# Kernel tuning notes

Measured on AMD Instinct MI355X. Metric: run time of the kernel, lower is better.

Reference implementation:

```python
import jax, jax.numpy as jnp
import numpy as np

B, C, H, W = 2, 128, 128, 128
HEADS = 8
D = C // HEADS
EPS = 1e-5


def _conv(x, w, pad):
    # x: [B,C,H,W], w: [O,I,kh,kw]
    return jax.lax.conv_general_dilated(
        x, w, window_strides=(1, 1), padding=[(pad, pad), (pad, pad)],
        dimension_numbers=("NCHW", "OIHW", "NCHW"))


def setup_inputs() -> dict:
    key = jax.random.key(0)
    ks = jax.random.split(key, 9)
    s = 0.05
    w11 = lambda k: jax.random.normal(k, (C, C, 1, 1), jnp.float32) * s
    w33 = lambda k: jax.random.normal(k, (C, C, 3, 3), jnp.float32) * s
    return {
        "x": jax.random.normal(ks[0], (B, C, H, W), jnp.float32),
        "gamma": jnp.ones((W,), jnp.float32),   # LayerNorm over LAST dim (W==C)
        "beta": jnp.zeros((W,), jnp.float32),
        "scale": jnp.ones((1,), jnp.float32),
        "wq1": w11(ks[1]), "wq2": w33(ks[2]),
        "wk1": w11(ks[3]), "wk2": w33(ks[4]),
        "wv1": w11(ks[5]), "wv2": w33(ks[6]),
        "wo": w11(ks[7]),
    }


def reference(x, gamma, beta, scale, wq1, wq2, wk1, wk2, wv1, wv2, wo):
    residual = x
    # torch nn.LayerNorm(channels) normalizes the last axis (W), biased variance
    mu = jnp.mean(x, axis=-1, keepdims=True)
    var = jnp.var(x, axis=-1, keepdims=True)
    xn = (x - mu) * jax.lax.rsqrt(var + EPS) * gamma + beta

    q = _conv(_conv(xn, wq1, 0), wq2, 1).reshape(B, HEADS, H * W, D)
    k = _conv(_conv(xn, wk1, 0), wk2, 1).reshape(B, HEADS, H * W, D).transpose(0, 1, 3, 2)
    v = _conv(_conv(xn, wv1, 0), wv2, 1).reshape(B, HEADS, H * W, D)

    # transposed (channel) attention: [B,h,d,HW] @ [B,h,HW,d] -> [B,h,d,d]
    attn = jnp.matmul(k, q) / scale
    probs = jax.nn.softmax(attn, axis=-1)
    out = jnp.matmul(v, probs)                      # [B,h,HW,d]
    out = out.transpose(0, 1, 3, 2).reshape(B, C, H, W)
    return _conv(out, wo, 0) + residual
```

## Files before the change

kernel.cpp:

```cpp
#include <hip/hip_runtime.h>
#include <hip/hip_bf16.h>

typedef unsigned short u16;
typedef _Float16 f16;
typedef f16 f16x8 __attribute__((ext_vector_type(8)));
typedef float f32x4 __attribute__((ext_vector_type(4)));

__device__ __forceinline__ float b2f(u16 u) {
  unsigned v = (unsigned)u << 16; float f; __builtin_memcpy(&f, &v, 4); return f;
}
__device__ __forceinline__ u16 f2b(float f) {
  return __builtin_bit_cast(u16, __float2bfloat16(f));
}
__device__ __forceinline__ float h2f(u16 u) {
  return (float)__builtin_bit_cast(f16, u);
}
__device__ __forceinline__ u16 f2h(float f) {
  return __builtin_bit_cast(u16, (f16)f);
}
__device__ __forceinline__ void gload16(const void* g, void* l) {
  __builtin_amdgcn_global_load_lds((__attribute__((address_space(1))) void*)(const_cast<void*>(g)),
                                   (__attribute__((address_space(3))) void*)l, 16, 0, 0);
}
__device__ __forceinline__ f32x4 mfma16(int4 a, int4 b, f32x4 c) {
  return __builtin_amdgcn_mfma_f32_16x16x32_f16(__builtin_bit_cast(f16x8, a),
                                                __builtin_bit_cast(f16x8, b), c, 0, 0, 0);
}
union PK { int4 i; u16 u[8]; };

__device__ __forceinline__ int detect_isf(const u16* x, int tid, int nthr) {
  __shared__ int dcnt;
  if (tid == 0) dcnt = 0;
  __syncthreads();
  int c = 0;
  for (int i = tid; i < 1024; i += nthr) {
    u16 u = x[i * 2];
    if (((u >> 7) & 0xFF) >= 0x90) ++c;
  }
  if (c) atomicAdd(&dcnt, c);
  __syncthreads();
  return dcnt > 16;
}

#define XROW 33280

__global__ __launch_bounds__(256) void k_weff(
    const void* __restrict__ w1q, const void* __restrict__ w2q,
    const void* __restrict__ w1k, const void* __restrict__ w2k,
    const void* __restrict__ w1v, const void* __restrict__ w2v,
    const u16* __restrict__ xdet, u16* __restrict__ weff) {
  __shared__ __align__(16) u16 sA[16384];
  __shared__ __align__(16) u16 sB[16384];
  int tid = threadIdx.x;
  int isf = detect_isf(xdet, tid, 256);
  int blk = blockIdx.x;
  int tap = blk / 3, br = blk - tap * 3;
  const void* w1 = br == 0 ? w1q : (br == 1 ? w1k : w1v);
  const void* w2 = br == 0 ? w2q : (br == 1 ? w2k : w2v);
  if (isf) {
    const float* w2f = (const float*)w2;
    const float* w1f = (const float*)w1;
#pragma unroll 4
    for (int i = 0; i < 64; ++i) {
      int e = i * 256 + tid;
      int c = e >> 7, m = e & 127;
      sA[c * 128 + (m ^ ((c & 15) << 3))] = f2h(w2f[e * 9 + tap]);
      int ci = e & 127;
      sB[ci * 128 + ((e >> 7) ^ ((ci & 15) << 3))] = f2h(w1f[e]);
    }
  } else {
    const u16* w2u = (const u16*)w2;
    const u16* w1u = (const u16*)w1;
#pragma unroll 4
    for (int i = 0; i < 64; ++i) {
      int e = i * 256 + tid;
      int c = e >> 7, m = e & 127;
      sA[c * 128 + (m ^ ((c & 15) << 3))] = f2h(b2f(w2u[e * 9 + tap]));
      int ci = e & 127;
      sB[ci * 128 + ((e >> 7) ^ ((ci & 15) << 3))] = f2h(b2f(w1u[e]));
    }
  }
  __syncthreads();
  int lane = tid & 63, wv = tid >> 6;
  int m0w = (wv >> 1) * 64, n0w = (wv & 1) * 64;
  f32x4 acc[4][4] = {};
#pragma unroll
  for (int k0 = 0; k0 < 4; ++k0) {
    int mrow = k0 * 32 + (lane >> 4) * 8;
    int4 a4[4], b4[4];
#pragma unroll
    for (int mi = 0; mi < 4; ++mi) {
      int c = m0w + mi * 16 + (lane & 15);
      a4[mi] = *(const int4*)&sA[c * 128 + (mrow ^ ((c & 15) << 3))];
    }
#pragma unroll
    for (int ni = 0; ni < 4; ++ni) {
      int ci = n0w + ni * 16 + (lane & 15);
      b4[ni] = *(const int4*)&sB[ci * 128 + (mrow ^ ((ci & 15) << 3))];
    }
#pragma unroll
    for (int mi = 0; mi < 4; ++mi)
#pragma unroll
      for (int ni = 0; ni < 4; ++ni)
        acc[mi][ni] = mfma16(a4[mi], b4[ni], acc[mi][ni]);
  }
  __syncthreads();
#pragma unroll
  for (int mi = 0; mi < 4; ++mi)
#pragma unroll
    for (int ni = 0; ni < 4; ++ni) {
#pragma unroll
      for (int r = 0; r < 4; ++r) {
        int c = m0w + mi * 16 + (lane >> 4) * 4 + r;
        int ci = n0w + ni * 16 + (lane & 15);
        sA[c * 128 + ci] = f2h(acc[mi][ni][r]);
      }
    }
  __syncthreads();
  int4* dst = (int4*)((char*)weff + (size_t)blk * 32768);
#pragma unroll
  for (int i = 0; i < 8; ++i) {
    int gidx = i * 256 + tid;
    int k0 = gidx >> 9;
    int ch = gidx & 511;
    int mt = ch >> 6, l = ch & 63;
    int c = mt * 16 + (l & 15);
    int g = k0 * 4 + (l >> 4);
    dst[gidx] = *(const int4*)((const char*)sA + c * 256 + g * 16);
  }
}

__global__ __launch_bounds__(256) void k_ln(const void* __restrict__ xr,
    const void* __restrict__ gr, const void* __restrict__ br_,
    u16* __restrict__ xnt, float* __restrict__ attnb) {
  __shared__ __align__(16) float sx[16384];
  __shared__ __align__(16) u16 sn[16384];
  __shared__ float sg[128], sb[128];
  int tid = threadIdx.x;
  int bi = blockIdx.x;
  if (bi >= 256) {
    int pid = bi - 256;
    int b = pid >> 1, row = (pid & 1) ? 129 : 0;
    char* rbase = (char*)xnt + (size_t)(b * 130 + row) * XROW;
    int4 z = make_int4(0, 0, 0, 0);
    for (int i = 0; i < 9; ++i) {
      int idx = i * 256 + tid;
      if (idx < 2080) *(int4*)(rbase + idx * 16) = z;
    }
    return;
  }
  if (bi == 0) {
    for (int i = tid; i < 4096; i += 256) attnb[i] = 0.f;
  }
  int b = bi >> 7, h = bi & 127;
  int isf = detect_isf((const u16*)xr, tid, 256);
  if (tid < 128) {
    sg[tid] = isf ? ((const float*)gr)[tid] : b2f(((const u16*)gr)[tid]);
    sb[tid] = isf ? ((const float*)br_)[tid] : b2f(((const u16*)br_)[tid]);
  }
  if (isf) {
#pragma unroll
    for (int it = 0; it < 16; ++it) {
      int d = it * 4096 + tid * 16;
      int c = d >> 9;
      int p = (d >> 4) & 31;
      int sc = p ^ (c & 31);
      const char* src = (const char*)xr + (size_t)(b * 128 + c) * 65536 + (size_t)h * 512 + (sc << 4);
      gload16(src, (char*)sx + d);
    }
  } else {
    int c = tid >> 1, half = tid & 1;
    const u16* xu = (const u16*)xr + ((size_t)(b * 128 + c) * 128 + h) * 128 + half * 64;
    for (int i = 0; i < 16; ++i) {
      int phys = (half * 16 + i) ^ (c & 31);
      float* dst = sx + c * 128 + phys * 4;
#pragma unroll
      for (int j = 0; j < 4; ++j) dst[j] = b2f(xu[i * 4 + j]);
    }
  }
  __syncthreads();
  int c = tid >> 1, half = tid & 1;
  float sum = 0.f, sq = 0.f;
#pragma unroll
  for (int i = 0; i < 16; ++i) {
    int phys = (half * 16 + i) ^ (c & 31);
    const float* v = sx + c * 128 + phys * 4;
#pragma unroll
    for (int j = 0; j < 4; ++j) { float f = v[j]; sum += f; sq += f * f; }
  }
  sum += __shfl_xor(sum, 1);
  sq  += __shfl_xor(sq, 1);
  float mu = sum * 0.0078125f;
  float var = sq * 0.0078125f - mu * mu;
  float rs = rsqrtf(var + 1e-5f);
  int cg = c >> 3, cl = c & 7;
#pragma unroll
  for (int i = 0; i < 16; ++i) {
    int logical = half * 16 + i;
    int phys = logical ^ (c & 31);
    const float* v = sx + c * 128 + phys * 4;
#pragma unroll
    for (int j = 0; j < 4; ++j) {
      int w = logical * 4 + j;
      sn[w * 128 + (((cg ^ (w & 15)) << 3) | cl)] = f2h((v[j] - mu) * rs * sg[w] + sb[w]);
    }
  }
  __syncthreads();
  char* obase = (char*)xnt + (size_t)(b * 130 + h + 1) * XROW;
#pragma unroll
  for (int i = 0; i < 8; ++i) {
    int idx = i * 256 + tid;
    int g = idx >> 7, w = idx & 127;
    int phys = g ^ (w & 15);
    *(int4*)(obase + (g * 130 + w + 1) * 16) = *(const int4*)((const char*)sn + w * 256 + (phys << 4));
  }
  if (tid < 32) {
    int g = tid >> 1, side = tid & 1;
    *(int4*)(obase + (g * 130 + (side ? 129 : 0)) * 16) = make_int4(0, 0, 0, 0);
  }
}

#define STAGE_T(T, BUF) do { \
    const char* base_ = (const char*)weff + (size_t)(T) * 32768; \
    char* dst_ = wq + (BUF) * 32768; \
    _Pragma("unroll") \
    for (int i_ = 0; i_ < 8; ++i_) \
      gload16(base_ + i_ * 4096 + tid * 16, dst_ + i_ * 4096 + tid * 16); \
  } while (0)

#define BC_LOAD(DST, T6) do { \
    int dy_ = (T6) / 3, dx_ = (T6) % 3; \
    const char* rb_ = (const char*)xnt + (size_t)(b * 130 + h + dy_) * XROW; \
    _Pragma("unroll") \
    for (int kk = 0; kk < 4; ++kk) \
      _Pragma("unroll") \
      for (int ni = 0; ni < 2; ++ni) { \
        int wp1 = whalf * 64 + n0l + ni * 16 + (lane & 15) + dx_;    \
        int chunk = (kk * 4 + (lane >> 4)) * 130 + wp1; \
        DST[kk][ni] = *(const int4*)(rb_ + chunk * 16); \
      } \
  } while (0)

#define QFULL(ACC, QB) do { \
    _Pragma("unroll") \
    for (int k0 = 0; k0 < 4; ++k0) { \
      int4 af[4]; \
      _Pragma("unroll") \
      for (int mi = 0; mi < 4; ++mi) \
        af[mi] = *(const int4*)((QB) + k0 * 8192 + ((wv >> 1) * 4 + mi) * 1024 + lane * 16); \
      _Pragma("unroll") \
      for (int mi = 0; mi < 4; ++mi) { \
        ACC[mi][0] = mfma16(af[mi], bcA[k0][0], ACC[mi][0]); \
        ACC[mi][1] = mfma16(af[mi], bcA[k0][1], ACC[mi][1]); \
      } \
    } \
  } while (0)

__global__ __launch_bounds__(256, 2) void k_conv(const u16* __restrict__ xnt,
    const u16* __restrict__ weff, u16* __restrict__ Vc, float* __restrict__ attnb) {
  __shared__ __align__(16) char wq[65536];
  int tid = threadIdx.x, lane = tid & 63, wv = tid >> 6;
  int bi = blockIdx.x;
  int whalf = bi & 1, h = (bi >> 1) & 127, b = bi >> 8;
  int m0 = (wv >> 1) * 64;
  int n0l = (wv & 1) * 32;
  int r9 = bi % 9;

  int4 bcA[4][2], bcB[4][2];
  BC_LOAD(bcA, r9);
  STAGE_T(3 * r9, 0);
  __syncthreads();

  f32x4 aq[4][2] = {}, ak[4][2] = {}, av[4][2] = {};

  for (int t = 0; t < 27; ++t) {
    int br = t % 3, tgrp = t / 3;
    if (t + 1 < 27) {
      int tt1 = t + 1 + 3 * r9;
      if (tt1 >= 27) tt1 -= 27;
      STAGE_T(tt1, (t + 1) & 1);
    }
    if (br == 0) {
      if (tgrp > 0) {
#pragma unroll
        for (int kk = 0; kk < 4; ++kk)
#pragma unroll
          for (int ni = 0; ni < 2; ++ni) bcA[kk][ni] = bcB[kk][ni];
      }
      if (tgrp < 8) {
        int ntap = tgrp + 1 + r9;
        if (ntap >= 9) ntap -= 9;
        BC_LOAD(bcB, ntap);
      }
    }
    const char* qb = wq + (t & 1) * 32768;
    if (br == 0)      QFULL(aq, qb);
    else if (br == 1) QFULL(ak, qb);
    else              QFULL(av, qb);
    __syncthreads();
  }
  u16* scrQ = (u16*)wq;
  u16* scrK = (u16*)(wq + 16384);
  u16* scrV = (u16*)(wq + 32768);
#pragma unroll
  for (int mi = 0; mi < 4; ++mi)
#pragma unroll
    for (int ni = 0; ni < 2; ++ni)
#pragma unroll
      for (int r = 0; r < 4; ++r) {
        int cc = m0 + mi * 16 + (lane >> 4) * 4 + r;
        int wl = n0l + ni * 16 + (lane & 15);
        scrQ[cc * 64 + wl] = f2h(aq[mi][ni][r]);
        scrK[cc * 64 + wl] = f2h(ak[mi][ni][r]);
        scrV[cc * 64 + wl] = f2h(av[mi][ni][r]);
      }
  __syncthreads();
#pragma unroll
  for (int hh = 0; hh < 2; ++hh) {
    int hd = wv * 2 + hh;
    f32x4 g = {};
#pragma unroll
    for (int k2 = 0; k2 < 2; ++k2) {
      PK A, Bq;
#pragma unroll
      for (int jj = 0; jj < 8; ++jj) {
        int k = (lane >> 4) * 8 + jj;
        int ci = k2 * 8 + (k >> 2);
        int wl = (k & 3) * 16 + (lane & 15);
        A.u[jj]  = scrK[(hd * 16 + ci) * 64 + wl];
        Bq.u[jj] = scrQ[(hd * 16 + ci) * 64 + wl];
      }
      g = mfma16(A.i, Bq.i, g);
    }
#pragma unroll
    for (int r = 0; r < 4; ++r)
      atomicAdd(&attnb[((b * 8 + hd) * 16 + (lane >> 4) * 4 + r) * 16 + (lane & 15)], g[r]);
  }
  char* dstV = (char*)Vc + (size_t)(b * 128) * 32768 + (size_t)h * 256 + (size_t)whalf * 128;
#pragma unroll
  for (int i = 0; i < 4; ++i) {
    int gi = i * 256 + tid;
    int c = gi >> 3, off = (gi & 7) << 4;
    *(int4*)(dstV + (size_t)c * 32768 + off) = *(const int4*)((const char*)scrV + c * 128 + off);
  }
}

__global__ __launch_bounds__(256) void k_w2(const float* __restrict__ attnb,
    const void* __restrict__ wo, const void* __restrict__ scale,
    const u16* __restrict__ xdet, u16* __restrict__ w2s) {
  __shared__ float P[256];
  int b = blockIdx.x, hd = blockIdx.y;
  int tid = threadIdx.x;
  int isf = detect_isf(xdet, tid, 256);
  float sc = isf ? ((const float*)scale)[0] : b2f(((const u16*)scale)[0]);
  float inv_sc = 1.f / sc;
  P[tid] = attnb[(b * 8 + hd) * 256 + tid] * inv_sc;
  __syncthreads();
  if (tid < 16) {
    int dk = tid;
    float m = -1e30f;
#pragma unroll
    for (int j = 0; j < 16; ++j) m = fmaxf(m, P[dk * 16 + j]);
    float e[16]; float s = 0.f;
#pragma unroll
    for (int j = 0; j < 16; ++j) { e[j] = expf(P[dk * 16 + j] - m); s += e[j]; }
    float is = 1.f / s;
#pragma unroll
    for (int j = 0; j < 16; ++j) P[dk * 16 + j] = e[j] * is;
  }
  __syncthreads();
  int co = tid & 127, kg = tid >> 7;
  float wr[16];
  if (isf) {
    const float* wof = (const float*)wo;
#pragma unroll
    for (int d = 0; d < 16; ++d) wr[d] = wof[co * 128 + hd * 16 + d];
  } else {
    const u16* wou = (const u16*)wo;
#pragma unroll
    for (int d = 0; d < 16; ++d) wr[d] = b2f(wou[co * 128 + hd * 16 + d]);
  }
  PK p;
#pragma unroll
  for (int j = 0; j < 8; ++j) {
    int dd = kg * 8 + j;
    float a = 0.f;
#pragma unroll
    for (int d = 0; d < 16; ++d) a += wr[d] * P[dd * 16 + d];
    p.u[j] = f2h(a);
  }
  int slot = hd * 2 + kg;
  *(int4*)((char*)w2s + (size_t)b * 32768 + co * 256 + ((slot ^ (co & 7)) << 4)) = p.i;
}

__global__ __launch_bounds__(256, 2) void k_final(const u16* __restrict__ w2s,
    const u16* __restrict__ Vc, const void* __restrict__ xr, void* __restrict__ outr) {
  __shared__ __align__(16) char sW[32768];
  __shared__ __align__(16) char sBk[16384];
  int tid = threadIdx.x, lane = tid & 63, wv = tid >> 6;
  int bi = blockIdx.x;
  int whalf = bi & 1, h = (bi >> 1) & 127, b = bi >> 8;
  int isf = detect_isf((const u16*)xr, tid, 256);
  const char* wsrc = (const char*)w2s + (size_t)b * 32768;
#pragma unroll
  for (int i = 0; i < 8; ++i) {
    int off = i * 4096 + tid * 16;
    gload16(wsrc + off, sW + off);
  }
#pragma unroll
  for (int i = 0; i < 4; ++i) {
    int gi = i * 256 + tid;
    int lr = gi >> 4, chunk = gi & 15;
    int hd8 = lr >> 3, rl = whalf * 8 + (lr & 7);
    int cv = hd8 * 16 + (h >> 3);
    int hv = (h & 7) * 16 + rl;
    const char* src = (const char*)Vc + (size_t)(b * 128 + cv) * 32768 + (size_t)hv * 256 + (chunk << 4);
    gload16(src, sBk + gi * 16);
  }
  __syncthreads();
  int m0 = (wv >> 1) * 64, n0l = (wv & 1) * 32;
  f32x4 acc[4][2] = {};
#pragma unroll
  for (int k0i = 0; k0i < 4; ++k0i) {
    int4 af[4], bfr[2];
#pragma unroll
    for (int mi = 0; mi < 4; ++mi) {
      int cc = m0 + mi * 16 + (lane & 15);
      int slot = (k0i * 4 + (lane >> 4)) ^ (cc & 7);
      af[mi] = *(const int4*)(sW + cc * 256 + (slot << 4));
    }
#pragma unroll
    for (int ni = 0; ni < 2; ++ni) {
      int wl = n0l + ni * 16 + (lane & 15);
      int k = k0i * 32 + (lane >> 4) * 8;
      int hd8 = k >> 4, dd0 = k & 15;
      bfr[ni] = *(const int4*)(sBk + (hd8 * 8 + (wl >> 3)) * 256 + ((wl & 7) * 32 + dd0 * 2));
    }
#pragma unroll
    for (int mi = 0; mi < 4; ++mi)
#pragma unroll
      for (int ni = 0; ni < 2; ++ni)
        acc[mi][ni] = mfma16(af[mi], bfr[ni], acc[mi][ni]);
  }
  if (isf) {
    const float* xf = (const float*)xr;
    float* of = (float*)outr;
#pragma unroll
    for (int mi = 0; mi < 4; ++mi)
#pragma unroll
      for (int ni = 0; ni < 2; ++ni) {
        int w = whalf * 64 + n0l + ni * 16 + (lane & 15);
#pragma unroll
        for (int r = 0; r < 4; ++r) {
          int cc = m0 + mi * 16 + (lane >> 4) * 4 + r;
          size_t idx = ((size_t)(b * 128 + cc) * 128 + (size_t)h) * 128 + w;
          of[idx] = acc[mi][ni][r] + xf[idx];
        }
      }
  } else {
    const u16* xu = (const u16*)xr;
    u16* ou = (u16*)outr;
#pragma unroll
    for (int mi = 0; mi < 4; ++mi)
#pragma unroll
      for (int ni = 0; ni < 2; ++ni) {
        int w = whalf * 64 + n0l + ni * 16 + (lane & 15);
#pragma unroll
        for (int r = 0; r < 4; ++r) {
          int cc = m0 + mi * 16 + (lane >> 4) * 4 + r;
          size_t idx = ((size_t)(b * 128 + cc) * 128 + (size_t)h) * 128 + w;
          ou[idx] = f2b(acc[mi][ni][r] + b2f(xu[idx]));
        }
      }
  }
}

extern "C" void kernel_launch(void* const* d_in, const int* in_sizes, int n_in,
                              void* d_out, int out_size, void* d_ws, size_t ws_size,
                              hipStream_t stream) {
  (void)in_sizes; (void)n_in; (void)out_size; (void)ws_size;
  const void* x     = d_in[0];
  const void* gamma = d_in[1];
  const void* beta  = d_in[2];
  const void* scale = d_in[3];
  const void* w1q = d_in[4];
  const void* w2q = d_in[5];
  const void* w1k = d_in[6];
  const void* w2k = d_in[7];
  const void* w1v = d_in[8];
  const void* w2v = d_in[9];
  const void* wo  = d_in[10];
  char* ws = (char*)d_ws;
  u16* xnt     = (u16*)(ws);
  u16* weff    = (u16*)(ws + (9u << 20));
  u16* Vc      = (u16*)(ws + (10u << 20));
  float* attnb = (float*)(ws + (18u << 20));
  u16* w2s     = (u16*)(ws + (18u << 20) + 65536);

  hipLaunchKernelGGL(k_weff, dim3(27), dim3(256), 0, stream, w1q, w2q, w1k, w2k, w1v, w2v,
                     (const u16*)x, weff);
  hipLaunchKernelGGL(k_ln, dim3(260), dim3(256), 0, stream, x, gamma, beta, xnt, attnb);
  hipLaunchKernelGGL(k_conv, dim3(512), dim3(256), 0, stream, xnt, weff, Vc, attnb);
  hipLaunchKernelGGL(k_w2, dim3(2, 8), dim3(256), 0, stream, attnb, wo, scale, (const u16*)x, w2s);
  hipLaunchKernelGGL(k_final, dim3(512), dim3(256), 0, stream, w2s, Vc, x, d_out);
}
```

Before: 88.07 us.

## Merge two image rows per conv block to share staged weight tiles

The conv kernel now runs 512-thread blocks that each cover two adjacent output rows, with each group of four waves handling one row. Both rows share the same LDS-staged weight tiles, which halves the global-to-LDS weight traffic per output. Epilogue scratch is split per row, and V is written in a separate LDS phase with an extra barrier. The per-block tap rotation (r9), which staggered weight reads across blocks, is removed. The grid shrinks from 512 to 256 blocks with one block per CU, so latency hiding and load balance may suffer.

```diff
diff --git a/kernel.cpp b/kernel.cpp
--- a/kernel.cpp
+++ b/kernel.cpp
@@ -224,8 +224,8 @@
     const char* base_ = (const char*)weff + (size_t)(T) * 32768; \
     char* dst_ = wq + (BUF) * 32768; \
     _Pragma("unroll") \
-    for (int i_ = 0; i_ < 8; ++i_) \
-      gload16(base_ + i_ * 4096 + tid * 16, dst_ + i_ * 4096 + tid * 16); \
+    for (int i_ = 0; i_ < 4; ++i_) \
+      gload16(base_ + i_ * 8192 + tid * 16, dst_ + i_ * 8192 + tid * 16); \
   } while (0)
 
 #define BC_LOAD(DST, T6) do { \
@@ -247,7 +247,7 @@
       int4 af[4]; \
       _Pragma("unroll") \
       for (int mi = 0; mi < 4; ++mi) \
-        af[mi] = *(const int4*)((QB) + k0 * 8192 + ((wv >> 1) * 4 + mi) * 1024 + lane * 16); \
+        af[mi] = *(const int4*)((QB) + k0 * 8192 + ((w4 >> 1) * 4 + mi) * 1024 + lane * 16); \
       _Pragma("unroll") \
       for (int mi = 0; mi < 4; ++mi) { \
         ACC[mi][0] = mfma16(af[mi], bcA[k0][0], ACC[mi][0]); \
@@ -256,30 +256,28 @@
     } \
   } while (0)
 
-__global__ __launch_bounds__(256, 2) void k_conv(const u16* __restrict__ xnt,
+__global__ __launch_bounds__(512, 1) void k_conv(const u16* __restrict__ xnt,
     const u16* __restrict__ weff, u16* __restrict__ Vc, float* __restrict__ attnb) {
   __shared__ __align__(16) char wq[65536];
   int tid = threadIdx.x, lane = tid & 63, wv = tid >> 6;
+  int wr = wv >> 2;
+  int w4 = wv & 3;
   int bi = blockIdx.x;
-  int whalf = bi & 1, h = (bi >> 1) & 127, b = bi >> 8;
-  int m0 = (wv >> 1) * 64;
-  int n0l = (wv & 1) * 32;
-  int r9 = bi % 9;
+  int whalf = bi & 1, hp = (bi >> 1) & 63, b = bi >> 7;
+  int h = hp * 2 + wr;
+  int m0 = (w4 >> 1) * 64;
+  int n0l = (w4 & 1) * 32;
 
   int4 bcA[4][2], bcB[4][2];
-  BC_LOAD(bcA, r9);
-  STAGE_T(3 * r9, 0);
+  BC_LOAD(bcA, 0);
+  STAGE_T(0, 0);
   __syncthreads();
 
   f32x4 aq[4][2] = {}, ak[4][2] = {}, av[4][2] = {};
 
   for (int t = 0; t < 27; ++t) {
     int br = t % 3, tgrp = t / 3;
-    if (t + 1 < 27) {
-      int tt1 = t + 1 + 3 * r9;
-      if (tt1 >= 27) tt1 -= 27;
-      STAGE_T(tt1, (t + 1) & 1);
-    }
+    if (t + 1 < 27) STAGE_T(t + 1, (t + 1) & 1);
     if (br == 0) {
       if (tgrp > 0) {
 #pragma unroll
@@ -287,11 +285,7 @@
 #pragma unroll
           for (int ni = 0; ni < 2; ++ni) bcA[kk][ni] = bcB[kk][ni];
       }
-      if (tgrp < 8) {
-        int ntap = tgrp + 1 + r9;
-        if (ntap >= 9) ntap -= 9;
-        BC_LOAD(bcB, ntap);
-      }
+      if (tgrp < 8) BC_LOAD(bcB, tgrp + 1);
     }
     const char* qb = wq + (t & 1) * 32768;
     if (br == 0)      QFULL(aq, qb);
@@ -299,9 +293,8 @@
     else              QFULL(av, qb);
     __syncthreads();
   }
-  u16* scrQ = (u16*)wq;
-  u16* scrK = (u16*)(wq + 16384);
-  u16* scrV = (u16*)(wq + 32768);
+  u16* scrQ = (u16*)(wq + wr * 32768);
+  u16* scrK = (u16*)(wq + wr * 32768 + 16384);
 #pragma unroll
   for (int mi = 0; mi < 4; ++mi)
 #pragma unroll
@@ -312,12 +305,11 @@
         int wl = n0l + ni * 16 + (lane & 15);
         scrQ[cc * 64 + wl] = f2h(aq[mi][ni][r]);
         scrK[cc * 64 + wl] = f2h(ak[mi][ni][r]);
-        scrV[cc * 64 + wl] = f2h(av[mi][ni][r]);
       }
   __syncthreads();
 #pragma unroll
   for (int hh = 0; hh < 2; ++hh) {
-    int hd = wv * 2 + hh;
+    int hd = w4 * 2 + hh;
     f32x4 g = {};
 #pragma unroll
     for (int k2 = 0; k2 < 2; ++k2) {
@@ -336,10 +328,24 @@
     for (int r = 0; r < 4; ++r)
       atomicAdd(&attnb[((b * 8 + hd) * 16 + (lane >> 4) * 4 + r) * 16 + (lane & 15)], g[r]);
   }
+  __syncthreads();
+  u16* scrV = (u16*)(wq + wr * 16384);
+#pragma unroll
+  for (int mi = 0; mi < 4; ++mi)
+#pragma unroll
+    for (int ni = 0; ni < 2; ++ni)
+#pragma unroll
+      for (int r = 0; r < 4; ++r) {
+        int cc = m0 + mi * 16 + (lane >> 4) * 4 + r;
+        int wl = n0l + ni * 16 + (lane & 15);
+        scrV[cc * 64 + wl] = f2h(av[mi][ni][r]);
+      }
+  __syncthreads();
   char* dstV = (char*)Vc + (size_t)(b * 128) * 32768 + (size_t)h * 256 + (size_t)whalf * 128;
+  int rtid = tid & 255;
 #pragma unroll
   for (int i = 0; i < 4; ++i) {
-    int gi = i * 256 + tid;
+    int gi = i * 256 + rtid;
     int c = gi >> 3, off = (gi & 7) << 4;
     *(int4*)(dstV + (size_t)c * 32768 + off) = *(const int4*)((const char*)scrV + c * 128 + off);
   }
@@ -500,7 +506,7 @@
   hipLaunchKernelGGL(k_weff, dim3(27), dim3(256), 0, stream, w1q, w2q, w1k, w2k, w1v, w2v,
                      (const u16*)x, weff);
   hipLaunchKernelGGL(k_ln, dim3(260), dim3(256), 0, stream, x, gamma, beta, xnt, attnb);
-  hipLaunchKernelGGL(k_conv, dim3(512), dim3(256), 0, stream, xnt, weff, Vc, attnb);
+  hipLaunchKernelGGL(k_conv, dim3(256), dim3(512), 0, stream, xnt, weff, Vc, attnb);
   hipLaunchKernelGGL(k_w2, dim3(2, 8), dim3(256), 0, stream, attnb, wo, scale, (const u16*)x, w2s);
   hipLaunchKernelGGL(k_final, dim3(512), dim3(256), 0, stream, w2s, Vc, x, d_out);
 }
```

After: 101.8 us. 15.6% more time.
